# Kernel optimization log

Measured on AMD Instinct MI355X. Metric: run time of the kernel, lower is better.

Reference implementation:

```python
import jax, jax.numpy as jnp
import numpy as np

EPS = 1e-5

def _sn(w):
    # spectral norm: divide by largest singular value of the (out,in) matrix
    return w / jnp.linalg.norm(w, ord=2)

def _conv1x1(w, b, x):
    # w: (O, C), x: (B, C, N) -> (B, O, N)
    return jnp.einsum('oc,bcn->bon', w, x) + b[None, :, None]

def _bn(x, g, be):
    # training-mode BatchNorm1d: stats over batch and length dims per channel
    m = jnp.mean(x, axis=(0, 2), keepdims=True)
    v = jnp.var(x, axis=(0, 2), keepdims=True)
    return (x - m) * jax.lax.rsqrt(v + EPS) * g[None, :, None] + be[None, :, None]

def setup_inputs() -> dict:
    key = jax.random.key(0)
    ks = jax.random.split(key, 10)
    B, N, H = 16, 2382, 8
    s = 0.1
    return {
        'z':  jax.random.normal(ks[0], (B, 1, N), jnp.float32),
        'w1': jax.random.normal(ks[1], (H, 1), jnp.float32) * s,
        'b1': jnp.zeros((H,), jnp.float32),
        'g1': jnp.ones((H,), jnp.float32),
        'be1': jnp.zeros((H,), jnp.float32),
        'wq': jax.random.normal(ks[2], (H // 8, H), jnp.float32) * s,
        'bq': jnp.zeros((H // 8,), jnp.float32),
        'wk': jax.random.normal(ks[3], (H // 8, H), jnp.float32) * s,
        'bk': jnp.zeros((H // 8,), jnp.float32),
        'wv': jax.random.normal(ks[4], (H, H), jnp.float32) * s,
        'bv': jnp.zeros((H,), jnp.float32),
        'gamma': jnp.float32(0.01),
        'w2': jax.random.normal(ks[5], (1, H), jnp.float32) * s,
        'b2': jnp.zeros((1,), jnp.float32),
        'g2': jnp.ones((1,), jnp.float32),
        'be2': jnp.zeros((1,), jnp.float32),
    }

def reference(z, w1, b1, g1, be1, wq, bq, wk, bk, wv, bv, gamma, w2, b2, g2, be2):
    # l1: SN-conv1x1 (1->H) + BN + ReLU
    x = jax.nn.relu(_bn(_conv1x1(_sn(w1), b1, z), g1, be1))        # (B, H, N)
    # SelfAttn: Q (B,N,1), K (B,1,N), V (B,H,N)
    Q = _conv1x1(_sn(wq), bq, x).transpose(0, 2, 1)                # (B, N, 1)
    K = _conv1x1(_sn(wk), bk, x)                                   # (B, 1, N)
    V = _conv1x1(_sn(wv), bv, x)                                   # (B, H, N)
    attn = jax.nn.softmax(jnp.einsum('bnc,bcm->bnm', Q, K), axis=-1)  # (B, N, N)
    out = jnp.einsum('bhm,bnm->bhn', V, attn)                      # V @ attn^T
    x = gamma * out + x
    # l2: SN-conv1x1 (H->1) + BN + ReLU
    x = jax.nn.relu(_bn(_conv1x1(_sn(w2), b2, x), g2, be2))        # (B, 1, N)
    return x
```

## Files before the change

kernel.cpp:

```cpp
#include <hip/hip_runtime.h>
#include <math.h>
#include <float.h>

#define BB 16
#define NN 2382
#define TOT 38112
#define NV4 9528
#define EPSF 1e-5f
#define L2E 1.4426950408889634f
#define TT 32
#define PITER 16
#define NB1 149

#define WS_KPQR 0
#define WS_TAB  152448
#define WS_META 152960
#define WS_MOM  153024

__global__ __launch_bounds__(256) void k1_kpqr(
    const float* __restrict__ z,  const float* __restrict__ w1,
    const float* __restrict__ g1, const float* __restrict__ be1,
    const float* __restrict__ wq, const float* __restrict__ bqp,
    const float* __restrict__ wk, const float* __restrict__ bkp,
    const float* __restrict__ wv, const float* __restrict__ bv,
    const float* __restrict__ w2, const float* __restrict__ b2p,
    float* __restrict__ ws)
{
    __shared__ float sred[8];
    const int tid = threadIdx.x;
    const int wave = tid >> 6, lane = tid & 63;

    const float4* __restrict__ z4 = (const float4*)z;
    float s = 0.f, s2 = 0.f;
    #pragma unroll 4
    for (int i = tid; i < NV4; i += 256) {
        const float4 v = z4[i];
        s += v.x + v.y + v.z + v.w;
        s2 = fmaf(v.x,v.x, fmaf(v.y,v.y, fmaf(v.z,v.z, fmaf(v.w,v.w, s2))));
    }
    #pragma unroll
    for (int off = 32; off; off >>= 1) {
        s  += __shfl_xor(s, off);
        s2 += __shfl_xor(s2, off);
    }
    if (lane == 0) { sred[wave] = s; sred[4+wave] = s2; }
    __syncthreads();
    const float invn = 1.f/(float)TOT;
    const float mz = (sred[0]+sred[1]+sred[2]+sred[3])*invn;
    const float vz = (sred[4]+sred[5]+sred[6]+sred[7])*invn - mz*mz;

    const int pi = lane >> 3, pj = lane & 7;
    float Mij = 0.f;
    #pragma unroll
    for (int o = 0; o < 8; ++o) Mij = fmaf(wv[o*8+pi], wv[o*8+pj], Mij);
    float u = 1.f, nr = 1.f;
    for (int it = 0; it < PITER; ++it) {
        float a = Mij*u;
        a += __shfl_xor(a,1); a += __shfl_xor(a,2); a += __shfl_xor(a,4);
        float bb = a*a;
        bb += __shfl_xor(bb,8); bb += __shfl_xor(bb,16); bb += __shfl_xor(bb,32);
        nr = sqrtf(bb);
        u = __shfl(a, pj<<3) / nr;
    }
    const float invsig = rsqrtf(nr);

    float n1=0.f, nq=0.f, nk=0.f, n2=0.f;
    #pragma unroll
    for (int h=0; h<8; ++h) {
        n1 = fmaf(w1[h], w1[h], n1);
        nq = fmaf(wq[h], wq[h], nq);
        nk = fmaf(wk[h], wk[h], nk);
        n2 = fmaf(w2[h], w2[h], n2);
    }
    n1 = sqrtf(n1); nq = sqrtf(nq); nk = sqrtf(nk); n2 = sqrtf(n2);

    float a1[8], c1[8], wqn[8], wkn[8], w2n[8], wvP[8];
    #pragma unroll
    for (int h=0; h<8; ++h) {
        const float w1n = w1[h]/n1;
        const float rs = rsqrtf(fmaf(w1n*w1n, vz, EPSF));
        a1[h]  = w1n * rs * g1[h];
        c1[h]  = be1[h] - mz*a1[h];
        wqn[h] = wq[h]/nq;
        wkn[h] = wk[h]/nk;
        w2n[h] = w2[h]/n2;
    }
    float bvP = 0.f;
    #pragma unroll
    for (int h=0; h<8; ++h) bvP = fmaf(w2n[h], bv[h], bvP);
    #pragma unroll
    for (int c=0; c<8; ++c) {
        float a = 0.f;
        #pragma unroll
        for (int h=0; h<8; ++h) a = fmaf(w2n[h], wv[h*8+c], a);
        wvP[c] = a * invsig;
    }

    const int item = blockIdx.x*256 + tid;
    if (item >= TOT) return;
    const float zv = z[item];
    float xh[8];
    #pragma unroll
    for (int h=0;h<8;++h) xh[h] = fmaxf(fmaf(a1[h], zv, c1[h]), 0.f);
    float kk = bkp[0], pp = bvP, qq = bqp[0], rr = b2p[0];
    #pragma unroll
    for (int h=0;h<8;++h) {
        kk = fmaf(wkn[h], xh[h], kk);
        pp = fmaf(wvP[h], xh[h], pp);
        qq = fmaf(wqn[h], xh[h], qq);
        rr = fmaf(w2n[h], xh[h], rr);
    }
    ((float4*)(ws + WS_KPQR))[item] = make_float4(kk, pp, qq, rr);
}

__global__ __launch_bounds__(1024) void k2_table(
    const float* __restrict__ ws_in, float* __restrict__ ws)
{
    __shared__ float2 sKP[NN];
    __shared__ float2 sQR[NN];
    __shared__ float  sG[TT];
    __shared__ float  sred[96];
    const int tid = threadIdx.x;
    const int wave = tid >> 6, lane = tid & 63;
    const int b = blockIdx.x;

    const float4* __restrict__ kpqr = (const float4*)(ws_in + WS_KPQR);
    float lkmax=-FLT_MAX, lkmin=FLT_MAX, lqmax=-FLT_MAX, lqmin=FLT_MAX;
    for (int n = tid; n < NN; n += 1024) {
        const float4 v = kpqr[b*NN + n];
        sKP[n] = make_float2(v.x, v.y);
        sQR[n] = make_float2(v.z, v.w);
        lkmax = fmaxf(lkmax, v.x); lkmin = fminf(lkmin, v.x);
        lqmax = fmaxf(lqmax, v.z); lqmin = fminf(lqmin, v.z);
    }
    #pragma unroll
    for (int off=32; off; off>>=1) {
        lkmax = fmaxf(lkmax, __shfl_xor(lkmax, off));
        lkmin = fminf(lkmin, __shfl_xor(lkmin, off));
        lqmax = fmaxf(lqmax, __shfl_xor(lqmax, off));
        lqmin = fminf(lqmin, __shfl_xor(lqmin, off));
    }
    if (lane == 0) {
        sred[wave] = lkmax; sred[16+wave] = lkmin;
        sred[32+wave] = lqmax; sred[48+wave] = lqmin;
    }
    __syncthreads();
    float kmax=-FLT_MAX, kmin=FLT_MAX, qmax=-FLT_MAX, qmin=FLT_MAX;
    #pragma unroll
    for (int j=0; j<16; ++j) {
        kmax = fmaxf(kmax, sred[j]);    kmin = fminf(kmin, sred[16+j]);
        qmax = fmaxf(qmax, sred[32+j]); qmin = fminf(qmin, sred[48+j]);
    }

    const int node = tid >> 5, sub = tid & 31;
    const float xq = fmaf((qmax-qmin), (float)node*(1.f/(float)(TT-1)), qmin);
    const float st = fmaxf(xq*kmax, xq*kmin);
    const float x2 = xq*L2E, st2 = st*L2E;
    float den = 0.f, num = 0.f;
    for (int m = sub; m < NN; m += 32) {
        const float2 kp = sKP[m];
        const float e = __builtin_amdgcn_exp2f(fmaf(x2, kp.x, -st2));
        den += e; num = fmaf(e, kp.y, num);
    }
    #pragma unroll
    for (int off=1; off<32; off<<=1) {
        den += __shfl_xor(den, off);
        num += __shfl_xor(num, off);
    }
    const float gnode = num/den;
    if (sub == 0) {
        sG[node] = gnode;
        ws[WS_TAB + b*TT + node] = gnode;
    }
    __syncthreads();

    const float qinv = (qmax > qmin) ? (float)(TT-1)/(qmax-qmin) : 0.f;
    float mG=0.f, mG2=0.f, mRG=0.f, mR=0.f, mR2=0.f;
    for (int n = tid; n < NN; n += 1024) {
        const float2 qr = sQR[n];
        float uu = fminf(fmaxf((qr.x - qmin)*qinv, 0.f), (float)(TT-1));
        int i = (int)uu; if (i > TT-2) i = TT-2;
        const float f = uu - (float)i;
        const float g = fmaf(f, sG[i+1]-sG[i], sG[i]);
        mG += g;            mG2 = fmaf(g, g, mG2);
        mRG = fmaf(qr.y, g, mRG);
        mR += qr.y;         mR2 = fmaf(qr.y, qr.y, mR2);
    }
    #pragma unroll
    for (int off=32; off; off>>=1) {
        mG  += __shfl_xor(mG,  off);
        mG2 += __shfl_xor(mG2, off);
        mRG += __shfl_xor(mRG, off);
        mR  += __shfl_xor(mR,  off);
        mR2 += __shfl_xor(mR2, off);
    }
    if (lane == 0) {
        sred[wave] = mG;     sred[16+wave] = mG2;  sred[32+wave] = mRG;
        sred[48+wave] = mR;  sred[64+wave] = mR2;
    }
    __syncthreads();
    if (tid == 0) {
        float tG=0.f, tG2=0.f, tRG=0.f, tR=0.f, tR2=0.f;
        #pragma unroll
        for (int j=0; j<16; ++j) {
            tG += sred[j]; tG2 += sred[16+j]; tRG += sred[32+j];
            tR += sred[48+j]; tR2 += sred[64+j];
        }
        ws[WS_MOM + b*5 + 0] = tG;
        ws[WS_MOM + b*5 + 1] = tG2;
        ws[WS_MOM + b*5 + 2] = tRG;
        ws[WS_MOM + b*5 + 3] = tR;
        ws[WS_MOM + b*5 + 4] = tR2;
        ws[WS_META + b*2]     = qmin;
        ws[WS_META + b*2 + 1] = qinv;
    }
}

__global__ __launch_bounds__(256) void k3_out(
    const float* __restrict__ ws, const float* __restrict__ gammap,
    const float* __restrict__ g2, const float* __restrict__ be2,
    float* __restrict__ out)
{
    const float gamma = gammap[0];
    float sy = 0.f, sy2 = 0.f;
    #pragma unroll
    for (int j = 0; j < BB; ++j) {
        const float tG  = ws[WS_MOM + j*5 + 0];
        const float tG2 = ws[WS_MOM + j*5 + 1];
        const float tRG = ws[WS_MOM + j*5 + 2];
        const float tR  = ws[WS_MOM + j*5 + 3];
        const float tR2 = ws[WS_MOM + j*5 + 4];
        sy  += tR + gamma*tG;
        sy2 += tR2 + 2.f*gamma*tRG + gamma*gamma*tG2;
    }
    const float invn = 1.f/(float)TOT;
    const float my = sy*invn;
    const float vy = sy2*invn - my*my;
    const float sc = g2[0]*rsqrtf(vy + EPSF);
    const float sh = be2[0] - my*sc;

    const int item = blockIdx.x*256 + threadIdx.x;
    if (item >= TOT) return;
    const int b = item / NN;
    const float4 v = ((const float4*)(ws + WS_KPQR))[item];
    const float qmin = ws[WS_META + b*2], qinv = ws[WS_META + b*2 + 1];
    float uu = fminf(fmaxf((v.z - qmin)*qinv, 0.f), (float)(TT-1));
    int i = (int)uu; if (i > TT-2) i = TT-2;
    const float f = uu - (float)i;
    const float g0 = ws[WS_TAB + b*TT + i];
    const float g1v = ws[WS_TAB + b*TT + i + 1];
    const float y = v.w + gamma*fmaf(f, g1v-g0, g0);
    out[item] = fmaxf(fmaf(y, sc, sh), 0.f);
}

extern "C" void kernel_launch(void* const* d_in, const int* in_sizes, int n_in,
                              void* d_out, int out_size, void* d_ws, size_t ws_size,
                              hipStream_t stream)
{
    const float* z    = (const float*)d_in[0];
    const float* w1   = (const float*)d_in[1];
    const float* g1   = (const float*)d_in[3];
    const float* be1  = (const float*)d_in[4];
    const float* wq   = (const float*)d_in[5];
    const float* bq   = (const float*)d_in[6];
    const float* wk   = (const float*)d_in[7];
    const float* bk   = (const float*)d_in[8];
    const float* wv   = (const float*)d_in[9];
    const float* bv   = (const float*)d_in[10];
    const float* gamma= (const float*)d_in[11];
    const float* w2   = (const float*)d_in[12];
    const float* b2   = (const float*)d_in[13];
    const float* g2   = (const float*)d_in[14];
    const float* be2  = (const float*)d_in[15];
    float* ws  = (float*)d_ws;
    float* out = (float*)d_out;

    k1_kpqr<<<NB1, 256, 0, stream>>>(
        z, w1, g1, be1, wq, bq, wk, bk, wv, bv, w2, b2, ws);

    k2_table<<<BB, 1024, 0, stream>>>(ws, ws);

    k3_out<<<NB1, 256, 0, stream>>>(ws, gamma, g2, be2, out);
}
```

Before: 28.14 us.

## Fuse per-element projection kernel into per-batch table kernel

Merges the first kernel, which computes K/P/Q/R per element, into the per-batch table kernel. Each of the 16 blocks now recomputes the global z statistics and the spectral-norm setup, then produces its batch's projections straight into shared memory. Only Q and R are written to the workspace as float2 for the output kernel, which cuts one launch and one global round trip. In exchange, every block repeats the full z-statistics reduction and power iteration redundantly, using only 16 blocks.

```diff
diff --git a/kernel.cpp b/kernel.cpp
--- a/kernel.cpp
+++ b/kernel.cpp
@@ -10,14 +10,14 @@
 #define L2E 1.4426950408889634f
 #define TT 32
 #define PITER 16
-#define NB1 149
-
-#define WS_KPQR 0
-#define WS_TAB  152448
-#define WS_META 152960
-#define WS_MOM  153024
-
-__global__ __launch_bounds__(256) void k1_kpqr(
+#define NB_OUT 149
+
+#define WS_QR   0
+#define WS_TAB  76288
+#define WS_META 76800
+#define WS_MOM  76864
+
+__global__ __launch_bounds__(1024) void kA_table(
     const float* __restrict__ z,  const float* __restrict__ w1,
     const float* __restrict__ g1, const float* __restrict__ be1,
     const float* __restrict__ wq, const float* __restrict__ bqp,
@@ -26,14 +26,17 @@
     const float* __restrict__ w2, const float* __restrict__ b2p,
     float* __restrict__ ws)
 {
-    __shared__ float sred[8];
+    __shared__ float2 sKP[NN];
+    __shared__ float2 sQR[NN];
+    __shared__ float  sG[TT];
+    __shared__ float  sred[96];
     const int tid = threadIdx.x;
     const int wave = tid >> 6, lane = tid & 63;
+    const int b = blockIdx.x;
 
     const float4* __restrict__ z4 = (const float4*)z;
     float s = 0.f, s2 = 0.f;
-    #pragma unroll 4
-    for (int i = tid; i < NV4; i += 256) {
+    for (int i = tid; i < NV4; i += 1024) {
         const float4 v = z4[i];
         s += v.x + v.y + v.z + v.w;
         s2 = fmaf(v.x,v.x, fmaf(v.y,v.y, fmaf(v.z,v.z, fmaf(v.w,v.w, s2))));
@@ -43,11 +46,15 @@
         s  += __shfl_xor(s, off);
         s2 += __shfl_xor(s2, off);
     }
-    if (lane == 0) { sred[wave] = s; sred[4+wave] = s2; }
+    if (lane == 0) { sred[wave] = s; sred[16+wave] = s2; }
     __syncthreads();
     const float invn = 1.f/(float)TOT;
-    const float mz = (sred[0]+sred[1]+sred[2]+sred[3])*invn;
-    const float vz = (sred[4]+sred[5]+sred[6]+sred[7])*invn - mz*mz;
+    float zs = 0.f, zq = 0.f;
+    #pragma unroll
+    for (int j = 0; j < 16; ++j) { zs += sred[j]; zq += sred[16+j]; }
+    const float mz = zs*invn;
+    const float vz = zq*invn - mz*mz;
+    __syncthreads();
 
     const int pi = lane >> 3, pj = lane & 7;
     float Mij = 0.f;
@@ -95,43 +102,29 @@
         for (int h=0; h<8; ++h) a = fmaf(w2n[h], wv[h*8+c], a);
         wvP[c] = a * invsig;
     }
-
-    const int item = blockIdx.x*256 + tid;
-    if (item >= TOT) return;
-    const float zv = z[item];
-    float xh[8];
-    #pragma unroll
-    for (int h=0;h<8;++h) xh[h] = fmaxf(fmaf(a1[h], zv, c1[h]), 0.f);
-    float kk = bkp[0], pp = bvP, qq = bqp[0], rr = b2p[0];
-    #pragma unroll
-    for (int h=0;h<8;++h) {
-        kk = fmaf(wkn[h], xh[h], kk);
-        pp = fmaf(wvP[h], xh[h], pp);
-        qq = fmaf(wqn[h], xh[h], qq);
-        rr = fmaf(w2n[h], xh[h], rr);
-    }
-    ((float4*)(ws + WS_KPQR))[item] = make_float4(kk, pp, qq, rr);
-}
-
-__global__ __launch_bounds__(1024) void k2_table(
-    const float* __restrict__ ws_in, float* __restrict__ ws)
-{
-    __shared__ float2 sKP[NN];
-    __shared__ float2 sQR[NN];
-    __shared__ float  sG[TT];
-    __shared__ float  sred[96];
-    const int tid = threadIdx.x;
-    const int wave = tid >> 6, lane = tid & 63;
-    const int b = blockIdx.x;
-
-    const float4* __restrict__ kpqr = (const float4*)(ws_in + WS_KPQR);
+    const float bq = bqp[0], bk = bkp[0], b2 = b2p[0];
+
+    const float* __restrict__ zb = z + b*NN;
+    float2* __restrict__ qr_out = (float2*)(ws + WS_QR);
     float lkmax=-FLT_MAX, lkmin=FLT_MAX, lqmax=-FLT_MAX, lqmin=FLT_MAX;
-    for (int n = tid; n < NN; n += 1024) {
-        const float4 v = kpqr[b*NN + n];
-        sKP[n] = make_float2(v.x, v.y);
-        sQR[n] = make_float2(v.z, v.w);
-        lkmax = fmaxf(lkmax, v.x); lkmin = fminf(lkmin, v.x);
-        lqmax = fmaxf(lqmax, v.z); lqmin = fminf(lqmin, v.z);
+    for (int m = tid; m < NN; m += 1024) {
+        const float zv = zb[m];
+        float xh[8];
+        #pragma unroll
+        for (int h=0;h<8;++h) xh[h] = fmaxf(fmaf(a1[h], zv, c1[h]), 0.f);
+        float kk = bk, pp = bvP, qq = bq, rr = b2;
+        #pragma unroll
+        for (int h=0;h<8;++h) {
+            kk = fmaf(wkn[h], xh[h], kk);
+            pp = fmaf(wvP[h], xh[h], pp);
+            qq = fmaf(wqn[h], xh[h], qq);
+            rr = fmaf(w2n[h], xh[h], rr);
+        }
+        sKP[m] = make_float2(kk, pp);
+        sQR[m] = make_float2(qq, rr);
+        qr_out[b*NN + m] = make_float2(qq, rr);
+        lkmax = fmaxf(lkmax, kk); lkmin = fminf(lkmin, kk);
+        lqmax = fmaxf(lqmax, qq); lqmin = fminf(lqmin, qq);
     }
     #pragma unroll
     for (int off=32; off; off>>=1) {
@@ -216,7 +209,7 @@
     }
 }
 
-__global__ __launch_bounds__(256) void k3_out(
+__global__ __launch_bounds__(256) void kB_out(
     const float* __restrict__ ws, const float* __restrict__ gammap,
     const float* __restrict__ g2, const float* __restrict__ be2,
     float* __restrict__ out)
@@ -242,14 +235,14 @@
     const int item = blockIdx.x*256 + threadIdx.x;
     if (item >= TOT) return;
     const int b = item / NN;
-    const float4 v = ((const float4*)(ws + WS_KPQR))[item];
+    const float2 qr = ((const float2*)(ws + WS_QR))[item];
     const float qmin = ws[WS_META + b*2], qinv = ws[WS_META + b*2 + 1];
-    float uu = fminf(fmaxf((v.z - qmin)*qinv, 0.f), (float)(TT-1));
+    float uu = fminf(fmaxf((qr.x - qmin)*qinv, 0.f), (float)(TT-1));
     int i = (int)uu; if (i > TT-2) i = TT-2;
     const float f = uu - (float)i;
     const float g0 = ws[WS_TAB + b*TT + i];
     const float g1v = ws[WS_TAB + b*TT + i + 1];
-    const float y = v.w + gamma*fmaf(f, g1v-g0, g0);
+    const float y = qr.y + gamma*fmaf(f, g1v-g0, g0);
     out[item] = fmaxf(fmaf(y, sc, sh), 0.f);
 }
 
@@ -275,10 +268,8 @@
     float* ws  = (float*)d_ws;
     float* out = (float*)d_out;
 
-    k1_kpqr<<<NB1, 256, 0, stream>>>(
+    kA_table<<<BB, 1024, 0, stream>>>(
         z, w1, g1, be1, wq, bq, wk, bk, wv, bv, w2, b2, ws);
 
-    k2_table<<<BB, 1024, 0, stream>>>(ws, ws);
-
-    k3_out<<<NB1, 256, 0, stream>>>(ws, gamma, g2, be2, out);
+    kB_out<<<NB_OUT, 256, 0, stream>>>(ws, gamma, g2, be2, out);
 }
```

New measurement: 28.72 us. 1.02x slower.

## Split pipeline into more parallel kernels for z-stats, table nodes and moments

Applied to the files above, without the earlier changes.

Moves the z mean and variance reduction into its own multi-block kernel, so the projection kernel no longer redundantly scans all of z in every block. Splits the softmax table build across a (node, batch) grid of 512 blocks, and the moment accumulation into a separate kernel, with per-block k and q ranges passed through the workspace. It also halves the power-iteration count for the spectral norm. In exchange it adds two extra kernel launches and global-memory round trips in place of shared-memory reuse.

```diff
diff --git a/kernel.cpp b/kernel.cpp
--- a/kernel.cpp
+++ b/kernel.cpp
@@ -9,15 +9,42 @@
 #define EPSF 1e-5f
 #define L2E 1.4426950408889634f
 #define TT 32
-#define PITER 16
-#define NB1 149
+#define PITER 8
+#define NXB 10
+#define NZB 38
+#define NB_OUT 149
 
 #define WS_KPQR 0
-#define WS_TAB  152448
-#define WS_META 152960
-#define WS_MOM  153024
-
-__global__ __launch_bounds__(256) void k1_kpqr(
+#define WS_ZS   152448
+#define WS_ZQ   152512
+#define WS_RNG  152576
+#define WS_TAB  153216
+#define WS_META 153728
+#define WS_MOM  153792
+
+__global__ __launch_bounds__(256) void n0_zstats(
+    const float* __restrict__ z, float* __restrict__ ws)
+{
+    __shared__ float sred[8];
+    const int tid = threadIdx.x, wave = tid >> 6, lane = tid & 63;
+    const int i = blockIdx.x*256 + tid;
+    float s = 0.f, s2 = 0.f;
+    if (i < NV4) {
+        const float4 v = ((const float4*)z)[i];
+        s  = v.x + v.y + v.z + v.w;
+        s2 = fmaf(v.x,v.x, fmaf(v.y,v.y, fmaf(v.z,v.z, v.w*v.w)));
+    }
+    #pragma unroll
+    for (int off=32; off; off>>=1){ s += __shfl_xor(s,off); s2 += __shfl_xor(s2,off); }
+    if (lane==0){ sred[wave]=s; sred[4+wave]=s2; }
+    __syncthreads();
+    if (tid==0) {
+        ws[WS_ZS+blockIdx.x] = sred[0]+sred[1]+sred[2]+sred[3];
+        ws[WS_ZQ+blockIdx.x] = sred[4]+sred[5]+sred[6]+sred[7];
+    }
+}
+
+__global__ __launch_bounds__(256) void n1_kpqr(
     const float* __restrict__ z,  const float* __restrict__ w1,
     const float* __restrict__ g1, const float* __restrict__ be1,
     const float* __restrict__ wq, const float* __restrict__ bqp,
@@ -26,28 +53,16 @@
     const float* __restrict__ w2, const float* __restrict__ b2p,
     float* __restrict__ ws)
 {
-    __shared__ float sred[8];
-    const int tid = threadIdx.x;
-    const int wave = tid >> 6, lane = tid & 63;
-
-    const float4* __restrict__ z4 = (const float4*)z;
-    float s = 0.f, s2 = 0.f;
-    #pragma unroll 4
-    for (int i = tid; i < NV4; i += 256) {
-        const float4 v = z4[i];
-        s += v.x + v.y + v.z + v.w;
-        s2 = fmaf(v.x,v.x, fmaf(v.y,v.y, fmaf(v.z,v.z, fmaf(v.w,v.w, s2))));
-    }
-    #pragma unroll
-    for (int off = 32; off; off >>= 1) {
-        s  += __shfl_xor(s, off);
-        s2 += __shfl_xor(s2, off);
-    }
-    if (lane == 0) { sred[wave] = s; sred[4+wave] = s2; }
-    __syncthreads();
+    __shared__ float sred[16];
+    const int tid = threadIdx.x, wave = tid >> 6, lane = tid & 63;
+    const int b = blockIdx.y;
+
+    float zs = 0.f, zq = 0.f;
+    #pragma unroll 2
+    for (int j=0; j<NZB; ++j) { zs += ws[WS_ZS+j]; zq += ws[WS_ZQ+j]; }
     const float invn = 1.f/(float)TOT;
-    const float mz = (sred[0]+sred[1]+sred[2]+sred[3])*invn;
-    const float vz = (sred[4]+sred[5]+sred[6]+sred[7])*invn - mz*mz;
+    const float mz = zs*invn;
+    const float vz = zq*invn - mz*mz;
 
     const int pi = lane >> 3, pj = lane & 7;
     float Mij = 0.f;
@@ -64,26 +79,26 @@
     }
     const float invsig = rsqrtf(nr);
 
-    float n1=0.f, nq=0.f, nk=0.f, n2=0.f;
+    float n1v=0.f, nqv=0.f, nkv=0.f, n2v=0.f;
     #pragma unroll
     for (int h=0; h<8; ++h) {
-        n1 = fmaf(w1[h], w1[h], n1);
-        nq = fmaf(wq[h], wq[h], nq);
-        nk = fmaf(wk[h], wk[h], nk);
-        n2 = fmaf(w2[h], w2[h], n2);
-    }
-    n1 = sqrtf(n1); nq = sqrtf(nq); nk = sqrtf(nk); n2 = sqrtf(n2);
+        n1v = fmaf(w1[h], w1[h], n1v);
+        nqv = fmaf(wq[h], wq[h], nqv);
+        nkv = fmaf(wk[h], wk[h], nkv);
+        n2v = fmaf(w2[h], w2[h], n2v);
+    }
+    n1v = sqrtf(n1v); nqv = sqrtf(nqv); nkv = sqrtf(nkv); n2v = sqrtf(n2v);
 
     float a1[8], c1[8], wqn[8], wkn[8], w2n[8], wvP[8];
     #pragma unroll
     for (int h=0; h<8; ++h) {
-        const float w1n = w1[h]/n1;
+        const float w1n = w1[h]/n1v;
         const float rs = rsqrtf(fmaf(w1n*w1n, vz, EPSF));
         a1[h]  = w1n * rs * g1[h];
         c1[h]  = be1[h] - mz*a1[h];
-        wqn[h] = wq[h]/nq;
-        wkn[h] = wk[h]/nk;
-        w2n[h] = w2[h]/n2;
+        wqn[h] = wq[h]/nqv;
+        wkn[h] = wk[h]/nkv;
+        w2n[h] = w2[h]/n2v;
     }
     float bvP = 0.f;
     #pragma unroll
@@ -96,42 +111,24 @@
         wvP[c] = a * invsig;
     }
 
-    const int item = blockIdx.x*256 + tid;
-    if (item >= TOT) return;
-    const float zv = z[item];
-    float xh[8];
-    #pragma unroll
-    for (int h=0;h<8;++h) xh[h] = fmaxf(fmaf(a1[h], zv, c1[h]), 0.f);
-    float kk = bkp[0], pp = bvP, qq = bqp[0], rr = b2p[0];
-    #pragma unroll
-    for (int h=0;h<8;++h) {
-        kk = fmaf(wkn[h], xh[h], kk);
-        pp = fmaf(wvP[h], xh[h], pp);
-        qq = fmaf(wqn[h], xh[h], qq);
-        rr = fmaf(w2n[h], xh[h], rr);
-    }
-    ((float4*)(ws + WS_KPQR))[item] = make_float4(kk, pp, qq, rr);
-}
-
-__global__ __launch_bounds__(1024) void k2_table(
-    const float* __restrict__ ws_in, float* __restrict__ ws)
-{
-    __shared__ float2 sKP[NN];
-    __shared__ float2 sQR[NN];
-    __shared__ float  sG[TT];
-    __shared__ float  sred[96];
-    const int tid = threadIdx.x;
-    const int wave = tid >> 6, lane = tid & 63;
-    const int b = blockIdx.x;
-
-    const float4* __restrict__ kpqr = (const float4*)(ws_in + WS_KPQR);
+    const int n = blockIdx.x*256 + tid;
+    float kk, pp, qq, rr;
     float lkmax=-FLT_MAX, lkmin=FLT_MAX, lqmax=-FLT_MAX, lqmin=FLT_MAX;
-    for (int n = tid; n < NN; n += 1024) {
-        const float4 v = kpqr[b*NN + n];
-        sKP[n] = make_float2(v.x, v.y);
-        sQR[n] = make_float2(v.z, v.w);
-        lkmax = fmaxf(lkmax, v.x); lkmin = fminf(lkmin, v.x);
-        lqmax = fmaxf(lqmax, v.z); lqmin = fminf(lqmin, v.z);
+    if (n < NN) {
+        const float zv = z[b*NN + n];
+        float xh[8];
+        #pragma unroll
+        for (int h=0;h<8;++h) xh[h] = fmaxf(fmaf(a1[h], zv, c1[h]), 0.f);
+        kk = bkp[0]; pp = bvP; qq = bqp[0]; rr = b2p[0];
+        #pragma unroll
+        for (int h=0;h<8;++h) {
+            kk = fmaf(wkn[h], xh[h], kk);
+            pp = fmaf(wvP[h], xh[h], pp);
+            qq = fmaf(wqn[h], xh[h], qq);
+            rr = fmaf(w2n[h], xh[h], rr);
+        }
+        ((float4*)(ws + WS_KPQR))[b*NN + n] = make_float4(kk, pp, qq, rr);
+        lkmax = kk; lkmin = kk; lqmax = qq; lqmin = qq;
     }
     #pragma unroll
     for (int off=32; off; off>>=1) {
@@ -141,50 +138,94 @@
         lqmin = fminf(lqmin, __shfl_xor(lqmin, off));
     }
     if (lane == 0) {
-        sred[wave] = lkmax; sred[16+wave] = lkmin;
-        sred[32+wave] = lqmax; sred[48+wave] = lqmin;
-    }
-    __syncthreads();
+        sred[wave]    = lkmax; sred[4+wave]  = lkmin;
+        sred[8+wave]  = lqmax; sred[12+wave] = lqmin;
+    }
+    __syncthreads();
+    if (tid == 0) {
+        const float kmax = fmaxf(fmaxf(sred[0],sred[1]), fmaxf(sred[2],sred[3]));
+        const float kmin = fminf(fminf(sred[4],sred[5]), fminf(sred[6],sred[7]));
+        const float qmax = fmaxf(fmaxf(sred[8],sred[9]), fmaxf(sred[10],sred[11]));
+        const float qmin = fminf(fminf(sred[12],sred[13]), fminf(sred[14],sred[15]));
+        ((float4*)(ws + WS_RNG))[b*NXB + blockIdx.x] =
+            make_float4(kmax, kmin, qmax, qmin);
+    }
+}
+
+__global__ __launch_bounds__(256) void n2_table(
+    const float* __restrict__ ws_in, float* __restrict__ ws)
+{
+    __shared__ float sred[8];
+    const int tid = threadIdx.x, wave = tid >> 6, lane = tid & 63;
+    const int node = blockIdx.x, b = blockIdx.y;
+
+    const float4* __restrict__ rng = (const float4*)(ws_in + WS_RNG);
     float kmax=-FLT_MAX, kmin=FLT_MAX, qmax=-FLT_MAX, qmin=FLT_MAX;
     #pragma unroll
-    for (int j=0; j<16; ++j) {
-        kmax = fmaxf(kmax, sred[j]);    kmin = fminf(kmin, sred[16+j]);
-        qmax = fmaxf(qmax, sred[32+j]); qmin = fminf(qmin, sred[48+j]);
-    }
-
-    const int node = tid >> 5, sub = tid & 31;
+    for (int j=0; j<NXB; ++j) {
+        const float4 r = rng[b*NXB + j];
+        kmax = fmaxf(kmax, r.x); kmin = fminf(kmin, r.y);
+        qmax = fmaxf(qmax, r.z); qmin = fminf(qmin, r.w);
+    }
     const float xq = fmaf((qmax-qmin), (float)node*(1.f/(float)(TT-1)), qmin);
     const float st = fmaxf(xq*kmax, xq*kmin);
     const float x2 = xq*L2E, st2 = st*L2E;
+
+    const float4* __restrict__ kpqr = (const float4*)(ws_in + WS_KPQR);
     float den = 0.f, num = 0.f;
-    for (int m = sub; m < NN; m += 32) {
-        const float2 kp = sKP[m];
-        const float e = __builtin_amdgcn_exp2f(fmaf(x2, kp.x, -st2));
-        den += e; num = fmaf(e, kp.y, num);
-    }
-    #pragma unroll
-    for (int off=1; off<32; off<<=1) {
+    #pragma unroll
+    for (int j = 0; j < NXB; ++j) {
+        const int m = j*256 + tid;
+        if (m < NN) {
+            const float4 v = kpqr[b*NN + m];
+            const float e = __builtin_amdgcn_exp2f(fmaf(x2, v.x, -st2));
+            den += e; num = fmaf(e, v.y, num);
+        }
+    }
+    #pragma unroll
+    for (int off=32; off; off>>=1) {
         den += __shfl_xor(den, off);
         num += __shfl_xor(num, off);
     }
-    const float gnode = num/den;
-    if (sub == 0) {
-        sG[node] = gnode;
-        ws[WS_TAB + b*TT + node] = gnode;
-    }
-    __syncthreads();
-
+    if (lane == 0) { sred[wave] = den; sred[4+wave] = num; }
+    __syncthreads();
+    if (tid == 0) {
+        const float d = sred[0]+sred[1]+sred[2]+sred[3];
+        const float nm = sred[4]+sred[5]+sred[6]+sred[7];
+        ws[WS_TAB + b*TT + node] = nm/d;
+    }
+}
+
+__global__ __launch_bounds__(1024) void n3_moments(
+    const float* __restrict__ ws_in, float* __restrict__ ws)
+{
+    __shared__ float sG[TT];
+    __shared__ float sred[80];
+    const int tid = threadIdx.x, wave = tid >> 6, lane = tid & 63;
+    const int b = blockIdx.x;
+
+    const float4* __restrict__ rng = (const float4*)(ws_in + WS_RNG);
+    float qmax=-FLT_MAX, qmin=FLT_MAX;
+    #pragma unroll
+    for (int j=0; j<NXB; ++j) {
+        const float4 r = rng[b*NXB + j];
+        qmax = fmaxf(qmax, r.z); qmin = fminf(qmin, r.w);
+    }
     const float qinv = (qmax > qmin) ? (float)(TT-1)/(qmax-qmin) : 0.f;
+    if (tid < TT) sG[tid] = ws_in[WS_TAB + b*TT + tid];
+    __syncthreads();
+
+    const float4* __restrict__ kpqr = (const float4*)(ws_in + WS_KPQR);
     float mG=0.f, mG2=0.f, mRG=0.f, mR=0.f, mR2=0.f;
     for (int n = tid; n < NN; n += 1024) {
-        const float2 qr = sQR[n];
-        float uu = fminf(fmaxf((qr.x - qmin)*qinv, 0.f), (float)(TT-1));
+        const float4 v = kpqr[b*NN + n];
+        float uu = fminf(fmaxf((v.z - qmin)*qinv, 0.f), (float)(TT-1));
         int i = (int)uu; if (i > TT-2) i = TT-2;
         const float f = uu - (float)i;
         const float g = fmaf(f, sG[i+1]-sG[i], sG[i]);
         mG += g;            mG2 = fmaf(g, g, mG2);
-        mRG = fmaf(qr.y, g, mRG);
-        mR += qr.y;         mR2 = fmaf(qr.y, qr.y, mR2);
+        mRG = fmaf(v.w, g, mRG);
+        mR += v.w;          mR2 = fmaf(v.w, v.w, mR2);
     }
     #pragma unroll
     for (int off=32; off; off>>=1) {
@@ -216,7 +257,7 @@
     }
 }
 
-__global__ __launch_bounds__(256) void k3_out(
+__global__ __launch_bounds__(256) void n4_out(
     const float* __restrict__ ws, const float* __restrict__ gammap,
     const float* __restrict__ g2, const float* __restrict__ be2,
     float* __restrict__ out)
@@ -275,10 +316,14 @@
     float* ws  = (float*)d_ws;
     float* out = (float*)d_out;
 
-    k1_kpqr<<<NB1, 256, 0, stream>>>(
+    n0_zstats<<<NZB, 256, 0, stream>>>(z, ws);
+
+    n1_kpqr<<<dim3(NXB, BB), 256, 0, stream>>>(
         z, w1, g1, be1, wq, bq, wk, bk, wv, bv, w2, b2, ws);
 
-    k2_table<<<BB, 1024, 0, stream>>>(ws, ws);
-
-    k3_out<<<NB1, 256, 0, stream>>>(ws, gamma, g2, be2, out);
-}
+    n2_table<<<dim3(TT, BB), 256, 0, stream>>>(ws, ws);
+
+    n3_moments<<<BB, 1024, 0, stream>>>(ws, ws);
+
+    n4_out<<<NB_OUT, 256, 0, stream>>>(ws, gamma, g2, be2, out);
+}
```

Result: no change. 28.49 us (+1.3%).
